# Optimization experiments

Measured on AMD Instinct MI355X. Metric: run time of the kernel, lower is better.

## Reference

```python
import jax, jax.numpy as jnp
import numpy as np
import itertools

DIM = 9  # LUT resolution per axis
B, C, H, W = 4, 5, 1024, 1024


def setup_inputs() -> dict:
    key = jax.random.key(0)
    k1, k2 = jax.random.split(key)
    x = jax.random.uniform(k1, (B, C, H, W), dtype=jnp.float32)  # pixel values in [0,1]
    LUT = jax.random.normal(k2, (1, 5, DIM, DIM, DIM, DIM, DIM), dtype=jnp.float32)
    return {"x": x, "LUT": LUT}


def _pglut_transform(x, LUT):
    # x: [B,5,H,W] in [0,1]; LUT: [1,5,dim,dim,dim,dim,dim]
    dim = LUT.shape[2]
    scale = jnp.float32(dim - 1)
    xs = x * scale                                   # [B,5,H,W]
    idx = jnp.clip(jnp.floor(xs), 0, dim - 2).astype(jnp.int32)
    frac = xs - idx.astype(x.dtype)                  # [B,5,H,W], in [0,1]

    lut_flat = LUT[0].reshape(5, dim ** 5)           # [5, dim^5]
    # flattened base index of the lower corner of the hypercube: [B,H,W]
    base = sum(idx[:, d] * int(dim ** (4 - d)) for d in range(5))

    out = jnp.zeros((5,) + base.shape, x.dtype)      # [5,B,H,W]
    for corner in itertools.product((0, 1), repeat=5):
        offset = sum(c * int(dim ** (4 - d)) for d, c in enumerate(corner))
        # quinlinear weight: prod_d (frac_d if corner else 1-frac_d)
        w = jnp.ones(base.shape, x.dtype)
        for d, c in enumerate(corner):
            w = w * (frac[:, d] if c else (1.0 - frac[:, d]))
        vals = lut_flat[:, base + offset]            # gather -> [5,B,H,W]
        out = out + w[None] * vals
    return jnp.transpose(out, (1, 0, 2, 3))          # [B,5,H,W]


def reference(x, LUT):
    return _pglut_transform(x, LUT)
```

## Files before the change

kernel.cpp:

```cpp
#include <hip/hip_runtime.h>
#include <hip/hip_fp16.h>


#define HW_    (1024 * 1024)
#define NPIX   (4 * HW_)
#define LUTC   59049
#define NBIN   512
#define CAP    8704
#define OVFCAP 65536
#define PXB    2048
#define NCELL2 (9 * 9 * 8 * 8 * 8)

#define R_BYTES   ((size_t)NCELL2 * 80)
#define PAY_ENT   ((size_t)NBIN * CAP + OVFCAP)
#define PAY_BYTES (PAY_ENT * 16)
#define POS_BYTES ((size_t)NPIX * 4)
#define OFF_R    ((size_t)0)
#define OFF_PAY  (OFF_R + R_BYTES)
#define OFF_POS  (OFF_PAY + PAY_BYTES)
#define OFF_CNT  (OFF_POS + POS_BYTES)
#define CNT_BYTES ((size_t)4096)
#define WS_NEED  (OFF_CNT + CNT_BYTES)

typedef _Float16 v2h __attribute__((ext_vector_type(2)));
union H2U { __half2 h; uint u; v2h v; };
union H8U { uint4 q; __half2 h2[4]; };
union HQ8 { __half h[8]; uint4 q; };

__global__ __launch_bounds__(256) void k1_buildR(
    const float* __restrict__ lut, __half* __restrict__ R)
{
    __shared__ float s[5 * 162];
    int bid = blockIdx.x;
    int i2 = bid & 7;
    int r  = bid >> 3;
    int Q  = r * 9 + i2;
    const int fb = Q * 81;
    for (int u = threadIdx.x; u < 5 * 162; u += 256) {
        int c = u / 162; int j = u - c * 162;
        s[u] = lut[(size_t)c * LUTC + fb + j];
    }
    __syncthreads();
    int cellBaseG = bid * 64;
    for (int t = threadIdx.x; t < 320; t += 256) {
        int cell = t / 5; int c = t - cell * 5;
        int i3 = cell >> 3, i4 = cell & 7;
        const float* L = s + c * 162 + i3 * 9 + i4;
        HQ8 u;
        u.h[0] = __float2half(L[0]);   u.h[1] = __float2half(L[81]);
        u.h[2] = __float2half(L[1]);   u.h[3] = __float2half(L[82]);
        u.h[4] = __float2half(L[9]);   u.h[5] = __float2half(L[90]);
        u.h[6] = __float2half(L[10]);  u.h[7] = __float2half(L[91]);
        ((uint4*)R)[(size_t)(cellBaseG + cell) * 5 + c] = u.q;
    }
}

__global__ __launch_bounds__(1024) void k4_fused(
    const float* __restrict__ x,
    uint* __restrict__ gcnt,
    uint4* __restrict__ pay, uint* __restrict__ sortpos)
{
    __shared__ uint4  sPay[PXB];
    __shared__ ushort sBin[PXB];
    __shared__ uint   sHist[NBIN];
    __shared__ uint   sCur[NBIN];
    __shared__ uint   sCB[NBIN];

    int tid = threadIdx.x, blk = blockIdx.x;
    if (tid < NBIN) sHist[tid] = 0;
    __syncthreads();

    uint4 plr[2]; uint keyr[2];
    #pragma unroll
    for (int kk = 0; kk < 2; ++kk) {
        int p = blk * PXB + kk * 1024 + tid;
        int b = p >> 20, hw = p & (HW_ - 1);
        const float* xp = x + (size_t)b * 5 * HW_ + hw;
        float f[5]; int idx[5];
        #pragma unroll
        for (int d = 0; d < 5; ++d) {
            float xs = __builtin_nontemporal_load(xp + (size_t)d * HW_) * 8.0f;
            int i = (int)floorf(xs); i = i < 0 ? 0 : (i > 7 ? 7 : i);
            idx[d] = i; f[d] = xs - (float)i;
        }
        int key   = (idx[0] << 6) | (idx[1] << 3) | idx[2];
        int local = (idx[3] << 3) | idx[4];
        H2U a, bq, c;
        a.h  = __float22half2_rn(make_float2(f[0], f[1]));
        bq.h = __float22half2_rn(make_float2(f[2], f[3]));
        c.h  = __float22half2_rn(make_float2(f[4], 0.f));
        plr[kk].x = a.u; plr[kk].y = bq.u; plr[kk].z = c.u;
        plr[kk].w = (uint)p | ((uint)local << 22);
        keyr[kk] = (uint)key;
        atomicAdd(&sHist[key], 1u);
    }
    __syncthreads();

    uint v = 0;
    if (tid < NBIN) { v = sHist[tid]; sCur[tid] = v; }
    __syncthreads();
    for (int off = 1; off < NBIN; off <<= 1) {
        uint t = 0;
        if (tid < NBIN && tid >= off) t = sCur[tid - off];
        __syncthreads();
        if (tid < NBIN) sCur[tid] += t;
        __syncthreads();
    }
    if (tid < NBIN) {
        sHist[tid] = sCur[tid] - v;
        uint base = 0;
        if (v) base = atomicAdd(&gcnt[tid], v);
        sCB[tid] = base;
    }
    __syncthreads();
    if (tid < NBIN) sCur[tid] = 0;
    __syncthreads();

    #pragma unroll
    for (int kk = 0; kk < 2; ++kk) {
        uint key  = keyr[kk];
        uint rank = atomicAdd(&sCur[key], 1u);
        uint slot = sHist[key] + rank;
        sPay[slot] = plr[kk];
        sBin[slot] = (ushort)key;
        uint gIdx = sCB[key] + rank;
        uint p    = plr[kk].w & 0x3FFFFFu;
        uint dst;
        if (gIdx < CAP) {
            dst = key * CAP + gIdx;
        } else {
            uint oi = atomicAdd(&gcnt[NBIN], 1u);
            if (oi >= OVFCAP) oi = OVFCAP - 1;
            pay[(size_t)NBIN * CAP + oi] = plr[kk];
            dst = (uint)(NBIN * CAP) + oi;
        }
        __builtin_nontemporal_store(dst, &sortpos[p]);
    }
    __syncthreads();

    for (int s = tid; s < PXB; s += 1024) {
        uint bin  = sBin[s];
        uint gIdx = sCB[bin] + ((uint)s - sHist[bin]);
        if (gIdx < CAP)
            pay[(size_t)bin * CAP + gIdx] = sPay[s];
    }
}

__global__ __launch_bounds__(256, 7) void k5_compute(
    const __half* __restrict__ R, const uint* __restrict__ gcnt,
    uint4* __restrict__ pay)
{
    __shared__ uint4 stbl[1280];
    int bid = blockIdx.x;
    int bin = bid >> 2, q = bid & 3;
    int i0 = bin >> 6, i1 = (bin >> 3) & 7, i2 = bin & 7;
    const uint4* R4 = (const uint4*)R;
    #pragma unroll
    for (int slab = 0; slab < 4; ++slab) {
        int a = slab >> 1, bcorner = slab & 1;
        size_t srcBase = (size_t)((((i0 + a) * 9 + (i1 + bcorner)) * 8 + i2) * 64) * 5;
        for (int rr = threadIdx.x; rr < 320; rr += 256)
            stbl[slab * 320 + rr] = R4[srcBase + rr];
    }
    __syncthreads();
    uint n = gcnt[bin]; if (n > CAP) n = CAP;
    uint B0 = (uint)bin * CAP;
    uint st = B0 + ((n * q) >> 2), en = B0 + ((n * (q + 1)) >> 2);
    for (uint i = st + threadIdx.x; i < en; i += 256) {
        uint4 pl = pay[i];
        H2U f01, f23, f4x; f01.u = pl.x; f23.u = pl.y; f4x.u = pl.z;
        float2 F01 = __half22float2(f01.h);
        float2 F23 = __half22float2(f23.h);
        float f0 = F01.x, f1 = F01.y, f2 = F23.x;
        __half2 f33 = __half2half2(__high2half(f23.h));
        __half2 f44 = __half2half2(__low2half(f4x.h));
        int local = (int)(pl.w >> 22);
        const uint4* cbase = stbl + local * 5;
        float g0 = 1.f - f0, g1 = 1.f - f1, g2 = 1.f - f2;
        H2U wv[4];
        float w00 = g0 * g1, w01c = g0 * f1, w10 = f0 * g1, w11 = f0 * f1;
        wv[0].h = __float22half2_rn(make_float2(w00  * g2, w00  * f2));
        wv[1].h = __float22half2_rn(make_float2(w01c * g2, w01c * f2));
        wv[2].h = __float22half2_rn(make_float2(w10  * g2, w10  * f2));
        wv[3].h = __float22half2_rn(make_float2(w11  * g2, w11  * f2));
        float acc[5];
        #pragma unroll
        for (int c = 0; c < 5; ++c) acc[c] = 0.f;
        #pragma unroll
        for (int slab = 0; slab < 4; ++slab) {
            #pragma unroll
            for (int c = 0; c < 5; ++c) {
                H8U u; u.q = cbase[slab * 320 + c];
                __half2 e0 = __hfma2(f44, __hsub2(u.h2[1], u.h2[0]), u.h2[0]);
                __half2 e1 = __hfma2(f44, __hsub2(u.h2[3], u.h2[2]), u.h2[2]);
                H2U dd; dd.h = __hfma2(f33, __hsub2(e1, e0), e0);
#if __has_builtin(__builtin_amdgcn_fdot2)
                acc[c] = __builtin_amdgcn_fdot2(dd.v, wv[slab].v, acc[c], false);
#else
                float2 D = __half22float2(dd.h);
                float2 W = __half22float2(wv[slab].h);
                acc[c] = fmaf(D.x, W.x, fmaf(D.y, W.y, acc[c]));
#endif
            }
        }
        H2U o01, o23, o4x;
        o01.h = __float22half2_rn(make_float2(acc[0], acc[1]));
        o23.h = __float22half2_rn(make_float2(acc[2], acc[3]));
        o4x.h = __float22half2_rn(make_float2(acc[4], 0.f));
        uint4 res; res.x = o01.u; res.y = o23.u; res.z = o4x.u; res.w = pl.w;
        pay[i] = res;
    }
}

__global__ __launch_bounds__(256) void k5_ovf(
    const float* __restrict__ x, const __half* __restrict__ R,
    const uint* __restrict__ gcnt, uint4* __restrict__ pay)
{
    uint n = gcnt[NBIN]; if (n > OVFCAP) n = OVFCAP;
    for (uint i = blockIdx.x * 256 + threadIdx.x; i < n; i += 64 * 256) {
        uint4 pl = pay[(size_t)NBIN * CAP + i];
        uint p = pl.w & 0x3FFFFFu;
        int b = p >> 20, hw = p & (HW_ - 1);
        const float* xp = x + (size_t)b * 5 * HW_ + hw;
        float f[5]; int idx[5];
        #pragma unroll
        for (int d = 0; d < 5; ++d) {
            float xs = xp[(size_t)d * HW_] * 8.0f;
            int ii = (int)floorf(xs); ii = ii < 0 ? 0 : (ii > 7 ? 7 : ii);
            idx[d] = ii; f[d] = xs - (float)ii;
        }
        float g0 = 1.f - f[0], g1 = 1.f - f[1];
        float f2 = f[2], f3 = f[3], f4 = f[4];
        int cellBase = ((idx[0] * 9 + idx[1]) * 8 + idx[2]) * 64 + idx[3] * 8 + idx[4];
        float acc[5];
        #pragma unroll
        for (int c = 0; c < 5; ++c) acc[c] = 0.f;
        #pragma unroll
        for (int c0 = 0; c0 < 2; ++c0) {
            float w0 = c0 ? f[0] : g0;
            int o0 = cellBase + c0 * 4608;
            #pragma unroll
            for (int c1 = 0; c1 < 2; ++c1) {
                float w = w0 * (c1 ? f[1] : g1);
                const uint4* pc = (const uint4*)R + (size_t)(o0 + c1 * 512) * 5;
                #pragma unroll
                for (int c = 0; c < 5; ++c) {
                    HQ8 u; u.q = pc[c];
                    float e00 = __half2float(u.h[0]) + f2 * (__half2float(u.h[1]) - __half2float(u.h[0]));
                    float e01 = __half2float(u.h[2]) + f2 * (__half2float(u.h[3]) - __half2float(u.h[2]));
                    float e10 = __half2float(u.h[4]) + f2 * (__half2float(u.h[5]) - __half2float(u.h[4]));
                    float e11 = __half2float(u.h[6]) + f2 * (__half2float(u.h[7]) - __half2float(u.h[6]));
                    float d0 = e00 + f4 * (e01 - e00);
                    float d1 = e10 + f4 * (e11 - e10);
                    float vv = d0 + f3 * (d1 - d0);
                    acc[c] = fmaf(w, vv, acc[c]);
                }
            }
        }
        H2U o01, o23, o4x;
        o01.h = __float22half2_rn(make_float2(acc[0], acc[1]));
        o23.h = __float22half2_rn(make_float2(acc[2], acc[3]));
        o4x.h = __float22half2_rn(make_float2(acc[4], 0.f));
        uint4 res; res.x = o01.u; res.y = o23.u; res.z = o4x.u; res.w = pl.w;
        pay[(size_t)NBIN * CAP + i] = res;
    }
}

__global__ __launch_bounds__(1024) void k6_unpermute(
    const uint* __restrict__ sortpos, const uint4* __restrict__ res,
    float* __restrict__ out)
{
    int p = blockIdx.x * 1024 + threadIdx.x;
    uint dst = sortpos[p];
    uint4 rr = res[dst];
    H2U a, bu, c; a.u = rr.x; bu.u = rr.y; c.u = rr.z;
    float2 v01 = __half22float2(a.h);
    float2 v23 = __half22float2(bu.h);
    float2 v4  = __half22float2(c.h);
    int b = p >> 20, hw = p & (HW_ - 1);
    float* op = out + (size_t)b * 5 * HW_ + hw;
    __builtin_nontemporal_store(v01.x, op);
    __builtin_nontemporal_store(v01.y, op + HW_);
    __builtin_nontemporal_store(v23.x, op + 2 * HW_);
    __builtin_nontemporal_store(v23.y, op + 3 * HW_);
    __builtin_nontemporal_store(v4.x,  op + 4 * HW_);
}

__global__ __launch_bounds__(256) void buildR3(
    const float* __restrict__ lut, __half* __restrict__ R)
{
    int t = blockIdx.x * blockDim.x + threadIdx.x;
    if (t >= 5 * NCELL2) return;
    int cell = t / 5;
    int c    = t - cell * 5;
    int i4 = cell & 7;
    int i3 = (cell >> 3) & 7;
    int i2 = (cell >> 6) & 7;
    int r  = cell >> 9;
    int i1 = r % 9;
    int i0 = r / 9;
    int flat = (((i0 * 9 + i1) * 9 + i2) * 9 + i3) * 9 + i4;
    const float* qq = lut + c * LUTC + flat;
    HQ8 u;
    u.h[0] = __float2half(qq[0]);  u.h[1] = __float2half(qq[1]);
    u.h[2] = __float2half(qq[9]);  u.h[3] = __float2half(qq[10]);
    u.h[4] = __float2half(qq[81]); u.h[5] = __float2half(qq[82]);
    u.h[6] = __float2half(qq[90]); u.h[7] = __float2half(qq[91]);
    ((uint4*)R)[t] = u.q;
}

__device__ __forceinline__ float lerpf(float a, float b, float t) {
    return fmaf(t, b - a, a);
}

__global__ __launch_bounds__(256) void gather3(
    const float* __restrict__ x, const __half* __restrict__ R,
    float* __restrict__ out)
{
    int p = blockIdx.x * blockDim.x + threadIdx.x;
    if (p >= NPIX) return;
    int b  = p >> 20;
    int hw = p & (HW_ - 1);
    const float* xp = x + (size_t)b * 5 * HW_ + hw;
    float f[5], g[5]; int idx[5];
    #pragma unroll
    for (int d = 0; d < 5; ++d) {
        float xs = __builtin_nontemporal_load(xp + (size_t)d * HW_) * 8.0f;
        int i = (int)floorf(xs); i = i < 0 ? 0 : (i > 7 ? 7 : i);
        idx[d] = i; f[d] = xs - (float)i; g[d] = 1.0f - f[d];
    }
    const float f2 = f[2], f3 = f[3], f4 = f[4];
    int base = ((idx[0] * 9 + idx[1]) * 8 + idx[2]) * 64 + idx[3] * 8 + idx[4];
    float acc0 = 0.f, acc1 = 0.f, acc2 = 0.f, acc3 = 0.f, acc4 = 0.f;
    #pragma unroll
    for (int c0 = 0; c0 < 2; ++c0) {
        const float w0 = c0 ? f[0] : g[0];
        const int  o0  = base + c0 * 4608;
        #pragma unroll
        for (int c1 = 0; c1 < 2; ++c1) {
            const float w  = w0 * (c1 ? f[1] : g[1]);
            const __half* pc = R + (size_t)(o0 + c1 * 512) * 40;
            #pragma unroll
            for (int c = 0; c < 5; ++c) {
                HQ8 u; u.q = *(const uint4*)(pc + c * 8);
                float v000 = __half2float(u.h[0]);
                float v001 = __half2float(u.h[1]);
                float v010 = __half2float(u.h[2]);
                float v011 = __half2float(u.h[3]);
                float v100 = __half2float(u.h[4]);
                float v101 = __half2float(u.h[5]);
                float v110 = __half2float(u.h[6]);
                float v111 = __half2float(u.h[7]);
                float e00 = lerpf(v000, v001, f2);
                float e01 = lerpf(v010, v011, f2);
                float e10 = lerpf(v100, v101, f2);
                float e11 = lerpf(v110, v111, f2);
                float d0  = lerpf(e00, e01, f4);
                float d1  = lerpf(e10, e11, f4);
                float s   = lerpf(d0, d1, f3);
                if      (c == 0) acc0 = fmaf(w, s, acc0);
                else if (c == 1) acc1 = fmaf(w, s, acc1);
                else if (c == 2) acc2 = fmaf(w, s, acc2);
                else if (c == 3) acc3 = fmaf(w, s, acc3);
                else             acc4 = fmaf(w, s, acc4);
            }
        }
    }
    float* op = out + (size_t)b * 5 * HW_ + hw;
    __builtin_nontemporal_store(acc0, op + 0 * HW_);
    __builtin_nontemporal_store(acc1, op + 1 * HW_);
    __builtin_nontemporal_store(acc2, op + 2 * HW_);
    __builtin_nontemporal_store(acc3, op + 3 * HW_);
    __builtin_nontemporal_store(acc4, op + 4 * HW_);
}

extern "C" void kernel_launch(void* const* d_in, const int* in_sizes, int n_in,
                              void* d_out, int out_size, void* d_ws, size_t ws_size,
                              hipStream_t stream)
{
    const float* x   = (const float*)d_in[0];
    const float* lut = (const float*)d_in[1];
    float* out       = (float*)d_out;
    char* ws         = (char*)d_ws;

    if (ws != nullptr && ws_size >= WS_NEED) {
        __half* R      = (__half*)(ws + OFF_R);
        uint4*  pay    = (uint4*)(ws + OFF_PAY);
        uint*   sortp  = (uint*)(ws + OFF_POS);
        uint*   gcnt   = (uint*)(ws + OFF_CNT);

        hipMemsetAsync(gcnt, 0, CNT_BYTES, stream);
        k1_buildR   <<<648, 256, 0, stream>>>(lut, R);
        k4_fused    <<<NPIX / PXB, 1024, 0, stream>>>(x, gcnt, pay, sortp);
        k5_compute  <<<4 * NBIN, 256, 0, stream>>>(R, gcnt, pay);
        k5_ovf      <<<64, 256, 0, stream>>>(x, R, gcnt, pay);
        k6_unpermute<<<NPIX / 1024, 1024, 0, stream>>>(sortp, pay, out);
    } else if (ws != nullptr && ws_size >= R_BYTES) {
        __half* R = (__half*)ws;
        int nb = (5 * NCELL2 + 255) / 256;
        buildR3<<<nb, 256, 0, stream>>>(lut, R);
        gather3<<<NPIX / 256, 256, 0, stream>>>(x, R, out);
    }
}
```

Baseline: 269.9 us.

## Restructure binning kernel: 512 threads, 4 pixels each, vector loads, wave-shuffle scan

The binning kernel now runs 512 threads per block, with each thread handling 4 consecutive pixels. Each thread reads x with 16-byte vector loads and writes sortpos as one uint4 store. The 9-step shared-memory prefix scan with many barriers becomes a wave-level shuffle scan plus a small cross-wave sum. Global bin counters are spaced two words apart, and the overflow counter moves to a separate slot, to reduce atomic contention and false sharing. The intent is fewer barriers and wider memory transactions, at the cost of more registers per thread and fewer threads to hide latency.

```diff
diff --git a/kernel.cpp b/kernel.cpp
--- a/kernel.cpp
+++ b/kernel.cpp
@@ -10,6 +10,7 @@
 #define OVFCAP 65536
 #define PXB    2048
 #define NCELL2 (9 * 9 * 8 * 8 * 8)
+#define OVF_IDX 1023
 
 #define R_BYTES   ((size_t)NCELL2 * 80)
 #define PAY_ENT   ((size_t)NBIN * CAP + OVFCAP)
@@ -23,6 +24,7 @@
 #define WS_NEED  (OFF_CNT + CNT_BYTES)
 
 typedef _Float16 v2h __attribute__((ext_vector_type(2)));
+typedef float    f4v __attribute__((ext_vector_type(4)));
 union H2U { __half2 h; uint u; v2h v; };
 union H8U { uint4 q; __half2 h2[4]; };
 union HQ8 { __half h[8]; uint4 q; };
@@ -55,31 +57,37 @@
     }
 }
 
-__global__ __launch_bounds__(1024) void k4_fused(
+__global__ __launch_bounds__(512) void k4_fused(
     const float* __restrict__ x,
     uint* __restrict__ gcnt,
     uint4* __restrict__ pay, uint* __restrict__ sortpos)
 {
     __shared__ uint4  sPay[PXB];
     __shared__ ushort sBin[PXB];
-    __shared__ uint   sHist[NBIN];
+    __shared__ uint   sStart[NBIN];
     __shared__ uint   sCur[NBIN];
     __shared__ uint   sCB[NBIN];
+    __shared__ uint   sWsum[8];
 
     int tid = threadIdx.x, blk = blockIdx.x;
-    if (tid < NBIN) sHist[tid] = 0;
-    __syncthreads();
-
-    uint4 plr[2]; uint keyr[2];
-    #pragma unroll
-    for (int kk = 0; kk < 2; ++kk) {
-        int p = blk * PXB + kk * 1024 + tid;
-        int b = p >> 20, hw = p & (HW_ - 1);
-        const float* xp = x + (size_t)b * 5 * HW_ + hw;
+    sCur[tid] = 0;
+    __syncthreads();
+
+    int pBase = blk * PXB + tid * 4;
+    int b = pBase >> 20, hw = pBase & (HW_ - 1);
+    const float* xp = x + (size_t)b * 5 * HW_ + hw;
+    f4v xv[5];
+    #pragma unroll
+    for (int d = 0; d < 5; ++d)
+        xv[d] = __builtin_nontemporal_load((const f4v*)(xp + (size_t)d * HW_));
+
+    uint4 plr[4]; uint keyr[4];
+    #pragma unroll
+    for (int j = 0; j < 4; ++j) {
         float f[5]; int idx[5];
         #pragma unroll
         for (int d = 0; d < 5; ++d) {
-            float xs = __builtin_nontemporal_load(xp + (size_t)d * HW_) * 8.0f;
+            float xs = xv[d][j] * 8.0f;
             int i = (int)floorf(xs); i = i < 0 ? 0 : (i > 7 ? 7 : i);
             idx[d] = i; f[d] = xs - (float)i;
         }
@@ -89,60 +97,61 @@
         a.h  = __float22half2_rn(make_float2(f[0], f[1]));
         bq.h = __float22half2_rn(make_float2(f[2], f[3]));
         c.h  = __float22half2_rn(make_float2(f[4], 0.f));
-        plr[kk].x = a.u; plr[kk].y = bq.u; plr[kk].z = c.u;
-        plr[kk].w = (uint)p | ((uint)local << 22);
-        keyr[kk] = (uint)key;
-        atomicAdd(&sHist[key], 1u);
-    }
-    __syncthreads();
-
-    uint v = 0;
-    if (tid < NBIN) { v = sHist[tid]; sCur[tid] = v; }
-    __syncthreads();
-    for (int off = 1; off < NBIN; off <<= 1) {
-        uint t = 0;
-        if (tid < NBIN && tid >= off) t = sCur[tid - off];
-        __syncthreads();
-        if (tid < NBIN) sCur[tid] += t;
-        __syncthreads();
-    }
-    if (tid < NBIN) {
-        sHist[tid] = sCur[tid] - v;
-        uint base = 0;
-        if (v) base = atomicAdd(&gcnt[tid], v);
-        sCB[tid] = base;
-    }
-    __syncthreads();
-    if (tid < NBIN) sCur[tid] = 0;
-    __syncthreads();
-
-    #pragma unroll
-    for (int kk = 0; kk < 2; ++kk) {
-        uint key  = keyr[kk];
+        plr[j].x = a.u; plr[j].y = bq.u; plr[j].z = c.u;
+        plr[j].w = (uint)(pBase + j) | ((uint)local << 22);
+        keyr[j] = (uint)key;
+        atomicAdd(&sCur[key], 1u);
+    }
+    __syncthreads();
+
+    uint v = sCur[tid];
+    uint base = 0;
+    if (v) base = atomicAdd(&gcnt[tid * 2], v);
+    uint s = v;
+    #pragma unroll
+    for (int off = 1; off < 64; off <<= 1) {
+        uint t = __shfl_up(s, off);
+        if ((tid & 63) >= off) s += t;
+    }
+    if ((tid & 63) == 63) sWsum[tid >> 6] = s;
+    __syncthreads();
+    uint add = 0;
+    #pragma unroll
+    for (int w = 0; w < 8; ++w)
+        add += (w < (tid >> 6)) ? sWsum[w] : 0u;
+    sStart[tid] = s + add - v;
+    sCB[tid]    = base;
+    sCur[tid]   = 0;
+    __syncthreads();
+
+    uint dstr[4];
+    #pragma unroll
+    for (int j = 0; j < 4; ++j) {
+        uint key  = keyr[j];
         uint rank = atomicAdd(&sCur[key], 1u);
-        uint slot = sHist[key] + rank;
-        sPay[slot] = plr[kk];
+        uint slot = sStart[key] + rank;
+        sPay[slot] = plr[j];
         sBin[slot] = (ushort)key;
         uint gIdx = sCB[key] + rank;
-        uint p    = plr[kk].w & 0x3FFFFFu;
         uint dst;
         if (gIdx < CAP) {
             dst = key * CAP + gIdx;
         } else {
-            uint oi = atomicAdd(&gcnt[NBIN], 1u);
+            uint oi = atomicAdd(&gcnt[OVF_IDX], 1u);
             if (oi >= OVFCAP) oi = OVFCAP - 1;
-            pay[(size_t)NBIN * CAP + oi] = plr[kk];
+            pay[(size_t)NBIN * CAP + oi] = plr[j];
             dst = (uint)(NBIN * CAP) + oi;
         }
-        __builtin_nontemporal_store(dst, &sortpos[p]);
-    }
-    __syncthreads();
-
-    for (int s = tid; s < PXB; s += 1024) {
-        uint bin  = sBin[s];
-        uint gIdx = sCB[bin] + ((uint)s - sHist[bin]);
+        dstr[j] = dst;
+    }
+    *(uint4*)(sortpos + pBase) = make_uint4(dstr[0], dstr[1], dstr[2], dstr[3]);
+    __syncthreads();
+
+    for (int sl = tid; sl < PXB; sl += 512) {
+        uint bin  = sBin[sl];
+        uint gIdx = sCB[bin] + ((uint)sl - sStart[bin]);
         if (gIdx < CAP)
-            pay[(size_t)bin * CAP + gIdx] = sPay[s];
+            pay[(size_t)bin * CAP + gIdx] = sPay[sl];
     }
 }
 
@@ -163,7 +172,7 @@
             stbl[slab * 320 + rr] = R4[srcBase + rr];
     }
     __syncthreads();
-    uint n = gcnt[bin]; if (n > CAP) n = CAP;
+    uint n = gcnt[bin * 2]; if (n > CAP) n = CAP;
     uint B0 = (uint)bin * CAP;
     uint st = B0 + ((n * q) >> 2), en = B0 + ((n * (q + 1)) >> 2);
     for (uint i = st + threadIdx.x; i < en; i += 256) {
@@ -216,7 +225,7 @@
     const float* __restrict__ x, const __half* __restrict__ R,
     const uint* __restrict__ gcnt, uint4* __restrict__ pay)
 {
-    uint n = gcnt[NBIN]; if (n > OVFCAP) n = OVFCAP;
+    uint n = gcnt[OVF_IDX]; if (n > OVFCAP) n = OVFCAP;
     for (uint i = blockIdx.x * 256 + threadIdx.x; i < n; i += 64 * 256) {
         uint4 pl = pay[(size_t)NBIN * CAP + i];
         uint p = pl.w & 0x3FFFFFu;
@@ -391,7 +400,7 @@
 
         hipMemsetAsync(gcnt, 0, CNT_BYTES, stream);
         k1_buildR   <<<648, 256, 0, stream>>>(lut, R);
-        k4_fused    <<<NPIX / PXB, 1024, 0, stream>>>(x, gcnt, pay, sortp);
+        k4_fused    <<<NPIX / PXB, 512, 0, stream>>>(x, gcnt, pay, sortp);
         k5_compute  <<<4 * NBIN, 256, 0, stream>>>(R, gcnt, pay);
         k5_ovf      <<<64, 256, 0, stream>>>(x, R, gcnt, pay);
         k6_unpermute<<<NPIX / 1024, 1024, 0, stream>>>(sortp, pay, out);
```

Measured after the change: 269.9 us. About the same (-0.0%).
